# Kernel optimization log

Measured on AMD Instinct MI355X. Metric: run time of the kernel, lower is better.

## Reference

```python
import jax, jax.numpy as jnp
import numpy as np
from jax import lax

B, L, C = 4, 4096, 512
H = 8           # head_num
D = C // H      # head dim = 64
RR = 4          # reduction_ratio -> reducer conv kernel 7, stride 4
KS = 3          # MixFFN depthwise kernel
ER = 4          # expansion ratio -> 2048 channels
EPS = 1e-5      # torch LayerNorm default eps


def _ln(x, g, b):
    # LayerNorm over last axis, affine per-channel
    m = jnp.mean(x, axis=-1, keepdims=True)
    v = jnp.mean(jnp.square(x - m), axis=-1, keepdims=True)
    return (x - m) * lax.rsqrt(v + EPS) * g + b


def setup_inputs() -> dict:
    key = jax.random.key(0)
    ks = jax.random.split(key, 9)
    s = lambda fan: 1.0 / np.sqrt(fan)
    return {
        "x": jax.random.normal(ks[0], (B, L, C), jnp.float32),
        "w_q": jax.random.normal(ks[1], (C, C), jnp.float32) * s(C),
        "w_k": jax.random.normal(ks[2], (C, C), jnp.float32) * s(C),
        "w_v": jax.random.normal(ks[3], (C, C), jnp.float32) * s(C),
        "w_o": jax.random.normal(ks[4], (C, C), jnp.float32) * s(C),
        "w_red": jax.random.normal(ks[5], (C, C, 2 * RR - 1), jnp.float32) * s(C * (2 * RR - 1)),
        "w_ffn1": jax.random.normal(ks[6], (C, C), jnp.float32) * s(C),
        "w_ffn_dw": jax.random.normal(ks[7], (C * ER, 1, KS), jnp.float32) * s(KS),
        "w_ffn2": jax.random.normal(ks[8], (C, C * ER), jnp.float32) * s(C * ER),
        "ln_gamma": jnp.ones((6, C), jnp.float32),
        "ln_beta": jnp.zeros((6, C), jnp.float32),
    }


def reference(x, w_q, w_k, w_v, w_o, w_red, w_ffn1, w_ffn_dw, w_ffn2, ln_gamma, ln_beta):
    # ln indices: 0=ln1(pre-attn), 1=ln(reducer), 2=ln_q, 3=ln_k, 4=ln_v, 5=ln2(pre-ffn)
    residual = x
    h = _ln(x, ln_gamma[0], ln_beta[0])  # B L C

    # --- spatial-reduction for K/V: reflect-pad strided conv + LN ---
    p = (2 * RR - 1) // 2
    hr = jnp.transpose(h, (0, 2, 1))  # B C L
    hr = jnp.pad(hr, ((0, 0), (0, 0), (p, p)), mode="reflect")
    red = lax.conv_general_dilated(hr, w_red, window_strides=(RR,), padding="VALID",
                                   dimension_numbers=("NCH", "OIH", "NCH"))  # B C Lr
    red = jnp.transpose(red, (0, 2, 1))  # B Lr C
    red = _ln(red, ln_gamma[1], ln_beta[1])

    # --- QKV projections + LayerNorms ---
    q = _ln(h @ w_q.T, ln_gamma[2], ln_beta[2])      # B L C
    k = _ln(red @ w_k.T, ln_gamma[3], ln_beta[3])    # B Lr C
    v = _ln(red @ w_v.T, ln_gamma[4], ln_beta[4])    # B Lr C

    Lr = k.shape[1]
    q = q.reshape(B, L, H, D).transpose(0, 2, 1, 3)   # B h L d
    k = k.reshape(B, Lr, H, D).transpose(0, 2, 1, 3)  # B h Lr d
    v = v.reshape(B, Lr, H, D).transpose(0, 2, 1, 3)

    scores = jnp.einsum("bhqd,bhkd->bhqk", q, k) / jnp.sqrt(jnp.float32(D))
    attn = jax.nn.softmax(scores, axis=-1)
    out = jnp.einsum("bhqk,bhkd->bhqd", attn, v)
    out = out.transpose(0, 2, 1, 3).reshape(B, L, C)
    out = out @ w_o.T

    h2 = out + residual
    residual2 = h2
    f = _ln(h2, ln_gamma[5], ln_beta[5])  # B L C

    # --- MixFFN: 1x1 conv -> depthwise reflect conv (groups=C, out=ER*C) -> GELU -> 1x1 conv ---
    f = jnp.transpose(f, (0, 2, 1))  # B C L
    f = jnp.einsum("oi,bil->bol", w_ffn1, f)  # 1x1, C->C
    pk = (KS - 1) // 2
    fp = jnp.pad(f, ((0, 0), (0, 0), (pk, pk)), mode="reflect")
    f = lax.conv_general_dilated(fp, w_ffn_dw, window_strides=(1,), padding="VALID",
                                 dimension_numbers=("NCH", "OIH", "NCH"),
                                 feature_group_count=C)  # B (ER*C) L
    f = jax.nn.gelu(f, approximate=False)  # torch nn.GELU() is exact erf
    f = jnp.einsum("oi,bil->bol", w_ffn2, f)  # 1x1, ER*C->C
    f = jnp.transpose(f, (0, 2, 1))  # B L C

    return f + residual2
```

## Files before the change

### kernel.cpp

```cpp
#include <hip/hip_runtime.h>
#include <math.h>

typedef __attribute__((ext_vector_type(8))) short short8;
typedef __attribute__((ext_vector_type(4))) short short4v;
typedef __attribute__((ext_vector_type(4))) float f32x4;
typedef unsigned short u16;
typedef unsigned int u32;
typedef unsigned long long u64;

namespace {
constexpr int kB = 4;
constexpr int kL = 4096;
constexpr int kC = 512;
constexpr int kH = 8;
constexpr int kLr = 1024;
constexpr int kCH = 2048;
constexpr int kKred = 3584;
constexpr float kEps = 1e-5f;
}

#if __has_builtin(__builtin_amdgcn_mfma_f32_16x16x16bf16_1k)
#define MFMA16X16(a, b, c) __builtin_amdgcn_mfma_f32_16x16x16bf16_1k((a), (b), (c), 0, 0, 0)
#else
__device__ __forceinline__ f32x4 mfma16_fb(short4v a, short4v b, f32x4 c) {
  asm volatile("v_mfma_f32_16x16x16_bf16 %0, %1, %2, %0\n\ts_nop 7\n\ts_nop 3"
               : "+v"(c) : "v"(a), "v"(b));
  return c;
}
#define MFMA16X16(a, b, c) mfma16_fb((a), (b), (c))
#endif

__device__ __forceinline__ float bf2f(u16 u) { return __uint_as_float(((u32)u) << 16); }
__device__ __forceinline__ u16 f2bf(float f) {
  u32 u = __float_as_uint(f);
  u32 r = (u + 0x7fffu + ((u >> 16) & 1u)) >> 16;
  return (u16)r;
}
__device__ __forceinline__ u32 cvtpk(float lo, float hi) {
  u32 r;
  asm("v_cvt_pk_bf16_f32 %0, %1, %2" : "=v"(r) : "v"(lo), "v"(hi));
  return r;
}
__device__ __forceinline__ float fexp2(float x) {
#if __has_builtin(__builtin_amdgcn_exp2f)
  return __builtin_amdgcn_exp2f(x);
#else
  float r;
  asm("v_exp_f32 %0, %1" : "=v"(r) : "v"(x));
  return r;
#endif
}

__device__ __forceinline__ void gload_lds16(const void* g, void* l) {
  __builtin_amdgcn_global_load_lds(
      (const __attribute__((address_space(1))) unsigned int*)g,
      (__attribute__((address_space(3))) unsigned int*)l, 16, 0, 0);
}

__device__ __forceinline__ short8 ldsfrag(const u16* base, int row, int col16) {
  return *(const short8*)(base + (size_t)(((row << 3) + (col16 ^ (row & 7))) << 3));
}

__global__ __launch_bounds__(256) void prep_weights_kernel(
    const float* __restrict__ w_q, const float* __restrict__ w_k,
    const float* __restrict__ w_v, const float* __restrict__ w_o,
    const float* __restrict__ w_f1, const float* __restrict__ w_f2,
    u16* __restrict__ dst, const float* __restrict__ w_red, u16* __restrict__ wredb) {
  if (blockIdx.x < 2304) {
    const int i = (blockIdx.x * 256 + threadIdx.x) * 4;
    const int seg = i >> 18;
    const float* src;
    int off;
    if (seg < 5) {
      src = (seg == 0) ? w_q : (seg == 1) ? w_k : (seg == 2) ? w_v : (seg == 3) ? w_o : w_f1;
      off = i & 262143;
    } else {
      src = w_f2;
      off = i - 1310720;
    }
    const float4 v = *(const float4*)(src + off);
    u16 o[4] = {f2bf(v.x), f2bf(v.y), f2bf(v.z), f2bf(v.w)};
    *(u64*)(dst + i) = *(u64*)o;
  } else {
    const int idx = (blockIdx.x - 2304) * 256 + threadIdx.x;
    if (idx >= kC * kKred) return;
    const int o = idx / kKred;
    const int rem = idx - o * kKred;
    const int t = rem >> 9;
    const int i = rem & (kC - 1);
    wredb[idx] = f2bf(w_red[(size_t)(o * kC + i) * 7 + t]);
  }
}

__global__ __launch_bounds__(256) void ln_bf16_kernel(const float* __restrict__ in,
                                                      u16* __restrict__ out,
                                                      const float* __restrict__ g,
                                                      const float* __restrict__ be) {
  const int row = blockIdx.x;
  const int tid = threadIdx.x;
  const float2 v = *(const float2*)(in + (size_t)row * kC + tid * 2);
  float s = v.x + v.y;
  float ss = v.x * v.x + v.y * v.y;
#pragma unroll
  for (int off = 32; off > 0; off >>= 1) {
    s += __shfl_down(s, off);
    ss += __shfl_down(ss, off);
  }
  __shared__ float wsum[4][2];
  __shared__ float mi[2];
  const int wave = tid >> 6, lane = tid & 63;
  if (lane == 0) { wsum[wave][0] = s; wsum[wave][1] = ss; }
  __syncthreads();
  if (tid == 0) {
    const float S = wsum[0][0] + wsum[1][0] + wsum[2][0] + wsum[3][0];
    const float SS = wsum[0][1] + wsum[1][1] + wsum[2][1] + wsum[3][1];
    const float mean = S * (1.0f / kC);
    const float var = SS * (1.0f / kC) - mean * mean;
    mi[0] = mean;
    mi[1] = rsqrtf(var + kEps);
  }
  __syncthreads();
  const float mean = mi[0], inv = mi[1];
  const float2 gg = *(const float2*)(g + tid * 2);
  const float2 bb = *(const float2*)(be + tid * 2);
  u16 o2[2] = {f2bf((v.x - mean) * inv * gg.x + bb.x), f2bf((v.y - mean) * inv * gg.y + bb.y)};
  *(u32*)(out + (size_t)row * kC + tid * 2) = *(u32*)o2;
}

__global__ __launch_bounds__(256) void reduce2_ln_kernel(const float* __restrict__ P,
                                                         u16* __restrict__ out,
                                                         const float* __restrict__ g,
                                                         const float* __restrict__ be) {
  const int row = blockIdx.x;
  const int tid = threadIdx.x;
  const size_t stride = (size_t)kB * kLr * kC;
  float2 v = make_float2(0.f, 0.f);
#pragma unroll
  for (int z = 0; z < 2; ++z) {
    const float2 p = *(const float2*)(P + z * stride + (size_t)row * kC + tid * 2);
    v.x += p.x;
    v.y += p.y;
  }
  float s = v.x + v.y;
  float ss = v.x * v.x + v.y * v.y;
#pragma unroll
  for (int off = 32; off > 0; off >>= 1) {
    s += __shfl_down(s, off);
    ss += __shfl_down(ss, off);
  }
  __shared__ float wsum[4][2];
  __shared__ float mi[2];
  const int wave = tid >> 6, lane = tid & 63;
  if (lane == 0) { wsum[wave][0] = s; wsum[wave][1] = ss; }
  __syncthreads();
  if (tid == 0) {
    const float S = wsum[0][0] + wsum[1][0] + wsum[2][0] + wsum[3][0];
    const float SS = wsum[0][1] + wsum[1][1] + wsum[2][1] + wsum[3][1];
    const float mean = S * (1.0f / kC);
    const float var = SS * (1.0f / kC) - mean * mean;
    mi[0] = mean;
    mi[1] = rsqrtf(var + kEps);
  }
  __syncthreads();
  const float mean = mi[0], inv = mi[1];
  const float2 gg = *(const float2*)(g + tid * 2);
  const float2 bb = *(const float2*)(be + tid * 2);
  u16 o2[2] = {f2bf((v.x - mean) * inv * gg.x + bb.x), f2bf((v.y - mean) * inv * gg.y + bb.y)};
  *(u32*)(out + (size_t)row * kC + tid * 2) = *(u32*)o2;
}

__global__ __launch_bounds__(256) void dwgelu_kernel(const u16* __restrict__ f1,
                                                     const float* __restrict__ wdw,
                                                     u16* __restrict__ fdw) {
  const int row = blockIdx.x;
  const int l = row & (kL - 1);
  const int rb = row - l;
  const int cc0 = threadIdx.x * 8;
  const int cg = cc0 >> 2;
  const int lm = (l == 0) ? 1 : l - 1;
  const int lp = (l == kL - 1) ? kL - 2 : l + 1;
  const u32 xm = *(const u32*)(f1 + (size_t)(rb + lm) * kC + cg);
  const u32 x0 = *(const u32*)(f1 + (size_t)(rb + l) * kC + cg);
  const u32 xp = *(const u32*)(f1 + (size_t)(rb + lp) * kC + cg);
  const float xml = bf2f((u16)xm), xmh = bf2f((u16)(xm >> 16));
  const float x0l = bf2f((u16)x0), x0h = bf2f((u16)(x0 >> 16));
  const float xpl = bf2f((u16)xp), xph = bf2f((u16)(xp >> 16));
  float wv[24];
#pragma unroll
  for (int t = 0; t < 6; ++t)
    *(float4*)&wv[t * 4] = *(const float4*)(wdw + (size_t)cc0 * 3 + t * 4);
  short8 pk;
#pragma unroll
  for (int j = 0; j < 8; ++j) {
    const float a_ = (j < 4) ? xml : xmh;
    const float b_ = (j < 4) ? x0l : x0h;
    const float c_ = (j < 4) ? xpl : xph;
    const float dw = wv[j * 3] * a_ + wv[j * 3 + 1] * b_ + wv[j * 3 + 2] * c_;
    pk[j] = (short)f2bf(0.5f * dw * (1.0f + erff(dw * 0.70710678118654752440f)));
  }
  *(short8*)(fdw + (size_t)row * kCH + cc0) = pk;
}

__global__ __launch_bounds__(256) void mgemm_red_kernel(
    const u16* __restrict__ A, const u16* __restrict__ W, float* __restrict__ OutF,
    int M, int N, int K) {
  __shared__ __align__(16) u16 As[2][128 * 64];
  __shared__ __align__(16) u16 Bs[2][128 * 64];
  const int tid = threadIdx.x;
  const int lane = tid & 63, w = tid >> 6;
  const int bid = blockIdx.x;
  const int m0 = (bid & 31) << 7, n0 = (bid >> 5) << 7;
  const int wm = (w >> 1) * 64, wn = (w & 1) * 64;
  const f32x4 zero = {0.f, 0.f, 0.f, 0.f};
  f32x4 acc[4][4];
#pragma unroll
  for (int i = 0; i < 4; ++i)
#pragma unroll
    for (int j = 0; j < 4; ++j) acc[i][j] = zero;

  const int kc = K / gridDim.z;
  const int kBeg = blockIdx.z * kc;
  float* outp = OutF + (size_t)blockIdx.z * M * N;

  auto stage = [&](int buf, int k0) {
#pragma unroll
    for (int c = 0; c < 4; ++c) {
      const int ci = w * 4 + c;
      const int idx = ci * 64 + lane;
      const int row = idx >> 3, s = idx & 7;
      const int c16 = s ^ (row & 7);
      gload_lds16(W + (size_t)(n0 + row) * K + k0 + c16 * 8, (char*)Bs[buf] + ci * 1024);
      const int m = m0 + row;
      const int b = m >> 10, lr = m & (kLr - 1);
      const int k = k0 + c16 * 8;
      const int t = k >> 9, i = k & (kC - 1);
      int pos = 4 * lr + t - 3;
      pos = pos < 0 ? -pos : (pos >= kL ? 2 * kL - 2 - pos : pos);
      gload_lds16(A + ((size_t)(b << 12) + pos) * kC + i, (char*)As[buf] + ci * 1024);
    }
  };

  const int nk = kc >> 6;
  stage(0, kBeg);
  __syncthreads();
  for (int t = 0; t < nk; ++t) {
    const int cur = t & 1;
    if (t + 1 < nk) stage(cur ^ 1, kBeg + ((t + 1) << 6));
#pragma unroll
    for (int kst = 0; kst < 2; ++kst) {
      short8 af[4], bfr[4];
      const int c16 = kst * 4 + (lane >> 4);
#pragma unroll
      for (int mb = 0; mb < 4; ++mb) af[mb] = ldsfrag(As[cur], wm + mb * 16 + (lane & 15), c16);
#pragma unroll
      for (int nb = 0; nb < 4; ++nb) bfr[nb] = ldsfrag(Bs[cur], wn + nb * 16 + (lane & 15), c16);
#pragma unroll
      for (int mb = 0; mb < 4; ++mb)
#pragma unroll
        for (int nb = 0; nb < 4; ++nb)
          acc[mb][nb] = __builtin_amdgcn_mfma_f32_16x16x32_bf16(af[mb], bfr[nb], acc[mb][nb], 0, 0, 0);
    }
    __syncthreads();
  }
#pragma unroll
  for (int mb = 0; mb < 4; ++mb)
#pragma unroll
    for (int r = 0; r < 4; ++r) {
      const int row = m0 + wm + mb * 16 + ((lane >> 4) << 2) + r;
#pragma unroll
      for (int nb = 0; nb < 4; ++nb)
        outp[(size_t)row * N + n0 + wn + nb * 16 + (lane & 15)] = acc[mb][nb][r];
    }
}

__global__ __launch_bounds__(256) void mgemm_res_kernel(
    const u16* __restrict__ A, const u16* __restrict__ W,
    const float* __restrict__ Res, float* __restrict__ OutF, int M, int N, int K) {
  __shared__ __align__(16) u16 As[2][128 * 64];
  __shared__ __align__(16) u16 Bs[2][128 * 64];
  const int tid = threadIdx.x;
  const int lane = tid & 63, w = tid >> 6;
  const int bid = blockIdx.x;
  const int m0 = (bid & 127) << 7, n0 = (bid >> 7) << 7;
  const int wm = (w >> 1) * 64, wn = (w & 1) * 64;
  const f32x4 zero = {0.f, 0.f, 0.f, 0.f};
  f32x4 acc[4][4];
#pragma unroll
  for (int i = 0; i < 4; ++i)
#pragma unroll
    for (int j = 0; j < 4; ++j) acc[i][j] = zero;

  auto stage = [&](int buf, int k0) {
#pragma unroll
    for (int c = 0; c < 4; ++c) {
      const int ci = w * 4 + c;
      const int idx = ci * 64 + lane;
      const int row = idx >> 3, s = idx & 7;
      const int c16 = s ^ (row & 7);
      gload_lds16(W + (size_t)(n0 + row) * K + k0 + c16 * 8, (char*)Bs[buf] + ci * 1024);
      gload_lds16(A + (size_t)(m0 + row) * K + k0 + c16 * 8, (char*)As[buf] + ci * 1024);
    }
  };

  const int nk = K >> 6;
  stage(0, 0);
  __syncthreads();
  for (int t = 0; t < nk; ++t) {
    const int cur = t & 1;
    if (t + 1 < nk) stage(cur ^ 1, (t + 1) << 6);
#pragma unroll
    for (int kst = 0; kst < 2; ++kst) {
      short8 af[4], bfr[4];
      const int c16 = kst * 4 + (lane >> 4);
#pragma unroll
      for (int mb = 0; mb < 4; ++mb) af[mb] = ldsfrag(As[cur], wm + mb * 16 + (lane & 15), c16);
#pragma unroll
      for (int nb = 0; nb < 4; ++nb) bfr[nb] = ldsfrag(Bs[cur], wn + nb * 16 + (lane & 15), c16);
#pragma unroll
      for (int mb = 0; mb < 4; ++mb)
#pragma unroll
        for (int nb = 0; nb < 4; ++nb)
          acc[mb][nb] = __builtin_amdgcn_mfma_f32_16x16x32_bf16(af[mb], bfr[nb], acc[mb][nb], 0, 0, 0);
    }
    __syncthreads();
  }
#pragma unroll
  for (int mb = 0; mb < 4; ++mb)
#pragma unroll
    for (int r = 0; r < 4; ++r) {
      const int row = m0 + wm + mb * 16 + ((lane >> 4) << 2) + r;
#pragma unroll
      for (int nb = 0; nb < 4; ++nb) {
        const size_t off = (size_t)row * N + n0 + wn + nb * 16 + (lane & 15);
        OutF[off] = acc[mb][nb][r] + Res[off];
      }
    }
}

template <int EPI>
__global__ __launch_bounds__(1024) void gemm512_kernel(
    const u16* __restrict__ A, const u16* __restrict__ W,
    const float* __restrict__ Res, float* __restrict__ OutF,
    u16* __restrict__ OutB, u16* __restrict__ OutB2,
    int K, const float* __restrict__ gam, const float* __restrict__ bet, float oscale) {
  constexpr bool RES_ = (EPI == 3);
  constexpr bool LN_ = (EPI == 1 || EPI == 2 || EPI == 3);
  constexpr int NMB = (EPI == 2) ? 1 : 2;
  constexpr int BM = NMB * 32;
  __shared__ __align__(16) u16 As[2][BM * 64];
  __shared__ __align__(16) u16 Bs[2][512 * 64];
  const int tid = threadIdx.x;
  const int lane = tid & 63, w = tid >> 6;
  const int l15 = lane & 15, g = lane >> 4;
  int bx, by;
  if (EPI == 2) { bx = blockIdx.x >> 7; by = blockIdx.x & 127; }
  else { bx = 0; by = blockIdx.x; }
  const int m0 = by * BM;
  const int n0 = bx * 512;
  const int wm = (w >> 3) * (NMB << 4);
  const int wn = (w & 7) << 6;
  const f32x4 zero = {0.f, 0.f, 0.f, 0.f};
  f32x4 acc[NMB][4];
#pragma unroll
  for (int i = 0; i < NMB; ++i)
#pragma unroll
    for (int j = 0; j < 4; ++j) acc[i][j] = zero;

  auto stage = [&](int buf, int k0) {
#pragma unroll
    for (int c = 0; c < 4; ++c) {
      const int cg = (w << 2) + c;
      const int idx = (cg << 6) + lane;
      const int row = idx >> 3, sl = idx & 7;
      const int c16 = sl ^ (row & 7);
      gload_lds16(W + (size_t)(n0 + row) * K + k0 + (c16 << 3), (char*)Bs[buf] + cg * 1024);
    }
    if (w < NMB * 4) {
      const int idx = (w << 6) + lane;
      const int row = idx >> 3, sl = idx & 7;
      const int c16 = sl ^ (row & 7);
      gload_lds16(A + (size_t)(m0 + row) * K + k0 + (c16 << 3), (char*)As[buf] + w * 1024);
    }
  };

  const int nk = K >> 6;
  stage(0, 0);
  __syncthreads();
  for (int t = 0; t < nk; ++t) {
    const int cur = t & 1;
    if (t + 1 < nk) stage(cur ^ 1, (t + 1) << 6);
#pragma unroll
    for (int kst = 0; kst < 2; ++kst) {
      const int c16 = (kst << 2) + g;
      short8 af[NMB], bfr[4];
#pragma unroll
      for (int mb = 0; mb < NMB; ++mb) af[mb] = ldsfrag(As[cur], wm + (mb << 4) + l15, c16);
#pragma unroll
      for (int nb = 0; nb < 4; ++nb) bfr[nb] = ldsfrag(Bs[cur], wn + (nb << 4) + l15, c16);
#pragma unroll
      for (int mb = 0; mb < NMB; ++mb)
#pragma unroll
        for (int nb = 0; nb < 4; ++nb)
          acc[mb][nb] = __builtin_amdgcn_mfma_f32_16x16x32_bf16(af[mb], bfr[nb], acc[mb][nb], 0, 0, 0);
    }
    __syncthreads();
  }

  if (RES_) {
#pragma unroll
    for (int mb = 0; mb < NMB; ++mb)
#pragma unroll
      for (int r = 0; r < 4; ++r) {
        const int grow = m0 + wm + (mb << 4) + (g << 2) + r;
#pragma unroll
        for (int nb = 0; nb < 4; ++nb)
          acc[mb][nb][r] += Res[(size_t)grow * kC + wn + (nb << 4) + l15];
      }
  }
  float* rs = (float*)As[0];
  float* rs2 = rs + 512;
  float2* minv = (float2*)(rs2 + 512);
  if (LN_) {
#pragma unroll
    for (int mb = 0; mb < NMB; ++mb)
#pragma unroll
      for (int r = 0; r < 4; ++r) {
        float s = acc[mb][0][r] + acc[mb][1][r] + acc[mb][2][r] + acc[mb][3][r];
        float s2 = acc[mb][0][r] * acc[mb][0][r] + acc[mb][1][r] * acc[mb][1][r] +
                   acc[mb][2][r] * acc[mb][2][r] + acc[mb][3][r] * acc[mb][3][r];
        s += __shfl_xor(s, 1); s += __shfl_xor(s, 2); s += __shfl_xor(s, 4); s += __shfl_xor(s, 8);
        s2 += __shfl_xor(s2, 1); s2 += __shfl_xor(s2, 2); s2 += __shfl_xor(s2, 4); s2 += __shfl_xor(s2, 8);
        if (l15 == 0) {
          const int rowf = wm + (mb << 4) + (g << 2) + r;
          rs[((w & 7) << 6) + rowf] = s;
          rs2[((w & 7) << 6) + rowf] = s2;
        }
      }
    __syncthreads();
    if (tid < BM) {
      float S = 0.f, SS = 0.f;
#pragma unroll
      for (int c8 = 0; c8 < 8; ++c8) { S += rs[(c8 << 6) + tid]; SS += rs2[(c8 << 6) + tid]; }
      const float mean = S * (1.0f / 512.0f);
      const float var = SS * (1.0f / 512.0f) - mean * mean;
      minv[tid] = make_float2(mean, rsqrtf(var + kEps));
    }
    __syncthreads();
  }
  float g4[4], b4[4];
  if (LN_) {
    const float* gp = (EPI == 2 && bx) ? gam + kC : gam;
    const float* bp = (EPI == 2 && bx) ? bet + kC : bet;
#pragma unroll
    for (int nb = 0; nb < 4; ++nb) {
      const int cc = wn + (nb << 4) + l15;
      g4[nb] = gp[cc];
      b4[nb] = bp[cc];
    }
  }
#pragma unroll
  for (int mb = 0; mb < NMB; ++mb) {
#pragma unroll
    for (int r = 0; r < 4; ++r) {
      const int rowf = wm + (mb << 4) + (g << 2) + r;
      const int grow = m0 + rowf;
      float2 mi = make_float2(0.f, 0.f);
      if (LN_) mi = minv[rowf];
#pragma unroll
      for (int nb = 0; nb < 4; ++nb) {
        const int cc = wn + (nb << 4) + l15;
        const float vv = acc[mb][nb][r];
        if (EPI == 0) {
          OutB[(size_t)grow * kC + cc] = f2bf(vv);
        } else if (EPI == 1) {
          OutB[(size_t)grow * kC + cc] = f2bf(((vv - mi.x) * mi.y * g4[nb] + b4[nb]) * oscale);
        } else if (EPI == 2) {
          const float lv = (vv - mi.x) * mi.y * g4[nb] + b4[nb];
          if (bx == 0) {
            OutB[(size_t)grow * kC + cc] = f2bf(lv);
          } else {
            const int b = grow >> 10, lr = grow & (kLr - 1);
            const int hh = cc >> 6, d = cc & 63;
            OutB2[((size_t)((b << 3) + hh) * 64 + d) * kLr + lr] = f2bf(lv);
          }
        } else {
          OutF[(size_t)grow * kC + cc] = vv;
          OutB[(size_t)grow * kC + cc] = f2bf((vv - mi.x) * mi.y * g4[nb] + b4[nb]);
        }
      }
    }
  }
}

__global__ __launch_bounds__(512, 4) void attn_mfma_kernel(
    const u16* __restrict__ q, const u16* __restrict__ k,
    const u16* __restrict__ vt, u16* __restrict__ o) {
  __shared__ __align__(16) u16 Ks[2][128 * 64];
  __shared__ __align__(16) char Vp[2][64 * 264];
  const int tid = threadIdx.x;
  const int lane = tid & 63, w = tid >> 6;
  const int bid = blockIdx.x;
  const int qt = bid >> 5;
  const int hb = bid & 31;
  const int h = hb >> 2, b = hb & 3;
  const int q0 = qt << 7;
  const int l15 = lane & 15, g = lane >> 4;

  short8 qf[2];
#pragma unroll
  for (int kst = 0; kst < 2; ++kst)
    qf[kst] = *(const short8*)(q + (size_t)((b << 12) + q0 + (w << 4) + l15) * kC +
                               (h << 6) + kst * 32 + g * 8);

  int kbase[2];
#pragma unroll
  for (int kst = 0; kst < 2; ++kst)
    kbase[kst] = (l15 << 7) + (((((kst << 2) + g) ^ (l15 & 7))) << 4);
  int voff[8];
#pragma unroll
  for (int nb = 0; nb < 8; ++nb) {
    const int chunk = (nb << 1) + (g >> 1);
    const int slot = chunk ^ (l15 & 7);
    voff[nb] = l15 * 264 + (slot << 4) + ((g & 1) << 3);
  }

  const int r_ = tid >> 3;
  const int sl_ = tid & 7;
  const int c16 = sl_ ^ (r_ & 7);
  const u16* kSrc = k + (size_t)((b << 10) + r_) * kC + (h << 6) + (c16 << 3);
  const u16* vSrc = vt + (size_t)(((b << 3) + h) * 64 + r_) * kLr + (c16 << 3);
  const int vdoff = r_ * 264 + (sl_ << 4);

  auto stageK = [&](int buf) {
    gload_lds16(kSrc, (char*)Ks[buf] + tid * 16);
    gload_lds16(kSrc + (size_t)64 * kC, (char*)Ks[buf] + 8192 + tid * 16);
  };

  stageK(0);
  kSrc += (size_t)128 * kC;
  {
    const float4 v0 = *(const float4*)vSrc;
    const float4 v1 = *(const float4*)(vSrc + 64);
    vSrc += 128;
    char* vd = Vp[0] + vdoff;
    *(float2*)(vd) = make_float2(v0.x, v0.y);
    *(float2*)(vd + 8) = make_float2(v0.z, v0.w);
    *(float2*)(vd + 128) = make_float2(v1.x, v1.y);
    *(float2*)(vd + 136) = make_float2(v1.z, v1.w);
  }

  const f32x4 zero = {0.f, 0.f, 0.f, 0.f};
  float l1 = 0.f;
  f32x4 accO[4] = {zero, zero, zero, zero};
  constexpr int nt = kLr / 128;

  __syncthreads();

  for (int t = 0; t < nt; ++t) {
    const int cur = t & 1;
    float4 vn0, vn1;
    if (t + 1 < nt) {
      vn0 = *(const float4*)vSrc;
      vn1 = *(const float4*)(vSrc + 64);
      vSrc += 128;
      stageK(cur ^ 1);
      kSrc += (size_t)128 * kC;
    }
    const char* kb = (const char*)Ks[cur];
    f32x4 st[8];
#pragma unroll
    for (int nb = 0; nb < 8; ++nb) st[nb] = zero;
    __builtin_amdgcn_s_setprio(1);
#pragma unroll
    for (int kst = 0; kst < 2; ++kst)
#pragma unroll
      for (int nb = 0; nb < 8; ++nb) {
        const short8 ak = *(const short8*)(kb + (nb << 11) + kbase[kst]);
        st[nb] = __builtin_amdgcn_mfma_f32_16x16x32_bf16(ak, qf[kst], st[nb], 0, 0, 0);
      }
    __builtin_amdgcn_s_setprio(0);
    short4v pa[8];
    {
      float ps = 0.f;
#pragma unroll
      for (int nb = 0; nb < 8; ++nb) {
#pragma unroll
        for (int r = 0; r < 4; ++r) {
          const float e = fexp2(st[nb][r]);
          st[nb][r] = e;
          ps += e;
        }
        u32 pw[2];
        pw[0] = cvtpk(st[nb][0], st[nb][1]);
        pw[1] = cvtpk(st[nb][2], st[nb][3]);
        pa[nb] = *(short4v*)pw;
      }
      l1 += ps;
    }
    const char* vbuf = Vp[cur];
    __builtin_amdgcn_s_setprio(1);
#pragma unroll
    for (int nb = 0; nb < 8; ++nb) {
#pragma unroll
      for (int d = 0; d < 4; ++d) {
        const short4v vb = *(const short4v*)(vbuf + voff[nb] + d * 4224);
        accO[d] = MFMA16X16(pa[nb], vb, accO[d]);
      }
    }
    __builtin_amdgcn_s_setprio(0);
    if (t + 1 < nt) {
      char* vd = Vp[cur ^ 1] + vdoff;
      *(float2*)(vd) = make_float2(vn0.x, vn0.y);
      *(float2*)(vd + 8) = make_float2(vn0.z, vn0.w);
      *(float2*)(vd + 128) = make_float2(vn1.x, vn1.y);
      *(float2*)(vd + 136) = make_float2(vn1.z, vn1.w);
    }
    __syncthreads();
  }
  l1 += __shfl_xor(l1, 16);
  l1 += __shfl_xor(l1, 32);
  float li[4];
#pragma unroll
  for (int r = 0; r < 4; ++r) li[r] = 1.0f / __shfl(l1, (g << 2) + r);
  const int qg = (b << 12) + q0 + (w << 4) + (g << 2);
#pragma unroll
  for (int d = 0; d < 4; ++d)
#pragma unroll
    for (int r = 0; r < 4; ++r)
      o[(size_t)(qg + r) * kC + (h << 6) + (d << 4) + l15] = f2bf(accO[d][r] * li[r]);
}

extern "C" void kernel_launch(void* const* d_in, const int* in_sizes, int n_in,
                              void* d_out, int out_size, void* d_ws, size_t ws_size,
                              hipStream_t stream) {
  const float* x      = (const float*)d_in[0];
  const float* w_q    = (const float*)d_in[1];
  const float* w_k    = (const float*)d_in[2];
  const float* w_v    = (const float*)d_in[3];
  const float* w_o    = (const float*)d_in[4];
  const float* w_red  = (const float*)d_in[5];
  const float* w_ffn1 = (const float*)d_in[6];
  const float* w_dw   = (const float*)d_in[7];
  const float* w_ffn2 = (const float*)d_in[8];
  const float* gam    = (const float*)d_in[9];
  const float* bet    = (const float*)d_in[10];
  float* out = (float*)d_out;

  const size_t nBLC = (size_t)kB * kL * kC;
  const size_t nBLrC = (size_t)kB * kLr * kC;
  u16* us = (u16*)d_ws;
  u16* wqb   = us;
  u16* wkb   = wqb + 262144;
  u16* wob   = wkb + 2 * 262144;
  u16* wf1b  = wob + 262144;
  u16* wf2b  = wf1b + 262144;
  u16* wredb = wf2b + 1048576;
  u16* h_b   = wredb + 1835008;
  u16* q_b   = h_b + nBLC;
  u16* red_b = q_b + nBLC;
  u16* k_b   = red_b + nBLrC;
  u16* vt_b  = k_b + nBLrC;
  float* S   = (float*)(vt_b + nBLrC);
  u16* fdw   = q_b;

  prep_weights_kernel<<<9472, 256, 0, stream>>>(w_q, w_k, w_v, w_o, w_ffn1, w_ffn2, wqb,
                                                w_red, wredb);

  ln_bf16_kernel<<<kB * kL, 256, 0, stream>>>(x, h_b, gam, bet);
  mgemm_red_kernel<<<dim3(128, 1, 2), 256, 0, stream>>>(h_b, wredb, S, kB * kLr, kC, kKred);
  reduce2_ln_kernel<<<kB * kLr, 256, 0, stream>>>(S, red_b, gam + kC, bet + kC);
  gemm512_kernel<1><<<dim3(256), 1024, 0, stream>>>(
      h_b, wqb, nullptr, nullptr, q_b, nullptr, kC, gam + 2 * kC, bet + 2 * kC,
      0.125f * 1.44269504088896f);
  gemm512_kernel<2><<<dim3(256), 1024, 0, stream>>>(
      red_b, wkb, nullptr, nullptr, k_b, vt_b, kC, gam + 3 * kC, bet + 3 * kC, 1.0f);
  attn_mfma_kernel<<<dim3(1024), 512, 0, stream>>>(q_b, k_b, vt_b, h_b);
  gemm512_kernel<3><<<dim3(256), 1024, 0, stream>>>(
      h_b, wob, x, out, q_b, nullptr, kC, gam + 5 * kC, bet + 5 * kC, 1.0f);
  gemm512_kernel<0><<<dim3(256), 1024, 0, stream>>>(
      q_b, wf1b, nullptr, nullptr, h_b, nullptr, kC, nullptr, nullptr, 1.0f);
  dwgelu_kernel<<<kB * kL, 256, 0, stream>>>(h_b, w_dw, fdw);
  mgemm_res_kernel<<<dim3(512), 256, 0, stream>>>(fdw, wf2b, out, out, kB * kL, kC, kCH);
}
```

Before: 261.2 us.

## Merge weight prep with first LayerNorm and double attention query tile per block

The first LayerNorm is folded into the weight-conversion kernel as extra blocks, removing one launch. The attention kernel now uses 1024 threads (16 waves) per block covering 256 queries, so each staged K/V tile is shared by twice as many query rows. Each thread now issues one K and one V load per tile instead of two. This halves K/V global traffic per query and the block count, but the larger blocks may strain registers and occupancy under the __launch_bounds__(1024, 8) hint.

```diff
diff --git a/kernel.cpp b/kernel.cpp
--- a/kernel.cpp
+++ b/kernel.cpp
@@ -61,13 +61,17 @@
   return *(const short8*)(base + (size_t)(((row << 3) + (col16 ^ (row & 7))) << 3));
 }
 
-__global__ __launch_bounds__(256) void prep_weights_kernel(
+__global__ __launch_bounds__(256) void prep_ln0_kernel(
     const float* __restrict__ w_q, const float* __restrict__ w_k,
     const float* __restrict__ w_v, const float* __restrict__ w_o,
     const float* __restrict__ w_f1, const float* __restrict__ w_f2,
-    u16* __restrict__ dst, const float* __restrict__ w_red, u16* __restrict__ wredb) {
-  if (blockIdx.x < 2304) {
-    const int i = (blockIdx.x * 256 + threadIdx.x) * 4;
+    u16* __restrict__ dst, const float* __restrict__ w_red, u16* __restrict__ wredb,
+    const float* __restrict__ x, u16* __restrict__ h_out,
+    const float* __restrict__ gam, const float* __restrict__ bet) {
+  const int bid = blockIdx.x;
+  const int tid = threadIdx.x;
+  if (bid < 2304) {
+    const int i = (bid * 256 + tid) * 4;
     const int seg = i >> 18;
     const float* src;
     int off;
@@ -81,24 +85,20 @@
     const float4 v = *(const float4*)(src + off);
     u16 o[4] = {f2bf(v.x), f2bf(v.y), f2bf(v.z), f2bf(v.w)};
     *(u64*)(dst + i) = *(u64*)o;
-  } else {
-    const int idx = (blockIdx.x - 2304) * 256 + threadIdx.x;
+    return;
+  }
+  if (bid < 9472) {
+    const int idx = (bid - 2304) * 256 + tid;
     if (idx >= kC * kKred) return;
     const int o = idx / kKred;
     const int rem = idx - o * kKred;
     const int t = rem >> 9;
     const int i = rem & (kC - 1);
     wredb[idx] = f2bf(w_red[(size_t)(o * kC + i) * 7 + t]);
-  }
-}
-
-__global__ __launch_bounds__(256) void ln_bf16_kernel(const float* __restrict__ in,
-                                                      u16* __restrict__ out,
-                                                      const float* __restrict__ g,
-                                                      const float* __restrict__ be) {
-  const int row = blockIdx.x;
-  const int tid = threadIdx.x;
-  const float2 v = *(const float2*)(in + (size_t)row * kC + tid * 2);
+    return;
+  }
+  const int row = bid - 9472;
+  const float2 v = *(const float2*)(x + (size_t)row * kC + tid * 2);
   float s = v.x + v.y;
   float ss = v.x * v.x + v.y * v.y;
 #pragma unroll
@@ -121,10 +121,10 @@
   }
   __syncthreads();
   const float mean = mi[0], inv = mi[1];
-  const float2 gg = *(const float2*)(g + tid * 2);
-  const float2 bb = *(const float2*)(be + tid * 2);
+  const float2 gg = *(const float2*)(gam + tid * 2);
+  const float2 bb = *(const float2*)(bet + tid * 2);
   u16 o2[2] = {f2bf((v.x - mean) * inv * gg.x + bb.x), f2bf((v.y - mean) * inv * gg.y + bb.y)};
-  *(u32*)(out + (size_t)row * kC + tid * 2) = *(u32*)o2;
+  *(u32*)(h_out + (size_t)row * kC + tid * 2) = *(u32*)o2;
 }
 
 __global__ __launch_bounds__(256) void reduce2_ln_kernel(const float* __restrict__ P,
@@ -492,7 +492,7 @@
   }
 }
 
-__global__ __launch_bounds__(512, 4) void attn_mfma_kernel(
+__global__ __launch_bounds__(1024, 8) void attn_mfma_kernel(
     const u16* __restrict__ q, const u16* __restrict__ k,
     const u16* __restrict__ vt, u16* __restrict__ o) {
   __shared__ __align__(16) u16 Ks[2][128 * 64];
@@ -503,7 +503,7 @@
   const int qt = bid >> 5;
   const int hb = bid & 31;
   const int h = hb >> 2, b = hb & 3;
-  const int q0 = qt << 7;
+  const int q0 = qt << 8;
   const int l15 = lane & 15, g = lane >> 4;
 
   short8 qf[2];
@@ -524,29 +524,28 @@
     voff[nb] = l15 * 264 + (slot << 4) + ((g & 1) << 3);
   }
 
-  const int r_ = tid >> 3;
-  const int sl_ = tid & 7;
-  const int c16 = sl_ ^ (r_ & 7);
-  const u16* kSrc = k + (size_t)((b << 10) + r_) * kC + (h << 6) + (c16 << 3);
-  const u16* vSrc = vt + (size_t)(((b << 3) + h) * 64 + r_) * kLr + (c16 << 3);
-  const int vdoff = r_ * 264 + (sl_ << 4);
-
-  auto stageK = [&](int buf) {
-    gload_lds16(kSrc, (char*)Ks[buf] + tid * 16);
-    gload_lds16(kSrc + (size_t)64 * kC, (char*)Ks[buf] + 8192 + tid * 16);
-  };
+  const int kr_ = tid >> 3;
+  const int ksl_ = tid & 7;
+  const int kc16 = ksl_ ^ (kr_ & 7);
+  const u16* kSrc = k + (size_t)((b << 10) + kr_) * kC + (h << 6) + (kc16 << 3);
+  const int rv_ = tid >> 4;
+  const int jv_ = tid & 15;
+  const int half_ = jv_ >> 3;
+  const int sv_ = jv_ & 7;
+  const int vc16 = sv_ ^ (rv_ & 7);
+  const u16* vSrc = vt + (size_t)(((b << 3) + h) * 64 + rv_) * kLr + half_ * 64 + (vc16 << 3);
+  const int vdoff = rv_ * 264 + half_ * 128 + (sv_ << 4);
+
+  auto stageK = [&](int buf) { gload_lds16(kSrc, (char*)Ks[buf] + tid * 16); };
 
   stageK(0);
   kSrc += (size_t)128 * kC;
   {
     const float4 v0 = *(const float4*)vSrc;
-    const float4 v1 = *(const float4*)(vSrc + 64);
     vSrc += 128;
     char* vd = Vp[0] + vdoff;
     *(float2*)(vd) = make_float2(v0.x, v0.y);
     *(float2*)(vd + 8) = make_float2(v0.z, v0.w);
-    *(float2*)(vd + 128) = make_float2(v1.x, v1.y);
-    *(float2*)(vd + 136) = make_float2(v1.z, v1.w);
   }
 
   const f32x4 zero = {0.f, 0.f, 0.f, 0.f};
@@ -558,10 +557,9 @@
 
   for (int t = 0; t < nt; ++t) {
     const int cur = t & 1;
-    float4 vn0, vn1;
+    float4 vn0;
     if (t + 1 < nt) {
       vn0 = *(const float4*)vSrc;
-      vn1 = *(const float4*)(vSrc + 64);
       vSrc += 128;
       stageK(cur ^ 1);
       kSrc += (size_t)128 * kC;
@@ -612,8 +610,6 @@
       char* vd = Vp[cur ^ 1] + vdoff;
       *(float2*)(vd) = make_float2(vn0.x, vn0.y);
       *(float2*)(vd + 8) = make_float2(vn0.z, vn0.w);
-      *(float2*)(vd + 128) = make_float2(vn1.x, vn1.y);
-      *(float2*)(vd + 136) = make_float2(vn1.z, vn1.w);
     }
     __syncthreads();
   }
@@ -663,10 +659,8 @@
   float* S   = (float*)(vt_b + nBLrC);
   u16* fdw   = q_b;
 
-  prep_weights_kernel<<<9472, 256, 0, stream>>>(w_q, w_k, w_v, w_o, w_ffn1, w_ffn2, wqb,
-                                                w_red, wredb);
-
-  ln_bf16_kernel<<<kB * kL, 256, 0, stream>>>(x, h_b, gam, bet);
+  prep_ln0_kernel<<<9472 + kB * kL, 256, 0, stream>>>(
+      w_q, w_k, w_v, w_o, w_ffn1, w_ffn2, wqb, w_red, wredb, x, h_b, gam, bet);
   mgemm_red_kernel<<<dim3(128, 1, 2), 256, 0, stream>>>(h_b, wredb, S, kB * kLr, kC, kKred);
   reduce2_ln_kernel<<<kB * kLr, 256, 0, stream>>>(S, red_b, gam + kC, bet + kC);
   gemm512_kernel<1><<<dim3(256), 1024, 0, stream>>>(
@@ -674,7 +668,7 @@
       0.125f * 1.44269504088896f);
   gemm512_kernel<2><<<dim3(256), 1024, 0, stream>>>(
       red_b, wkb, nullptr, nullptr, k_b, vt_b, kC, gam + 3 * kC, bet + 3 * kC, 1.0f);
-  attn_mfma_kernel<<<dim3(1024), 512, 0, stream>>>(q_b, k_b, vt_b, h_b);
+  attn_mfma_kernel<<<dim3(512), 1024, 0, stream>>>(q_b, k_b, vt_b, h_b);
   gemm512_kernel<3><<<dim3(256), 1024, 0, stream>>>(
       h_b, wob, x, out, q_b, nullptr, kC, gam + 5 * kC, bet + 5 * kC, 1.0f);
   gemm512_kernel<0><<<dim3(256), 1024, 0, stream>>>(
```

Result: slower. 381.5 us (+46.0%).
